# Optimization experiments

Measured on AMD Instinct MI355X. Metric: run time of the kernel, lower is better.

The kernel has to match this reference:

```python
import jax, jax.numpy as jnp
import numpy as np

B, S, D = 8, 2048, 64
NEG = -1e9


def setup_inputs() -> dict:
    key = jax.random.key(0)
    kq, kk, kv = jax.random.split(key, 3)
    return {
        "queries": jax.random.normal(kq, (B, S, D), dtype=jnp.float32),
        "keys": jax.random.normal(kk, (B, S, D), dtype=jnp.float32),
        "values": jax.random.normal(kv, (B, S, D), dtype=jnp.float32),
        "mask_q": jnp.ones((B, S), dtype=jnp.float32),
        "mask_k": jnp.ones((B, S), dtype=jnp.float32),
        "mask_v": jnp.ones((B, S), dtype=jnp.float32),
    }


def reference(queries, keys, values, mask_q, mask_k, mask_v):
    # scaled QK^T: [B, Sq, Sk]
    scaler = jnp.sqrt(jnp.asarray(queries.shape[-1], dtype=queries.dtype))
    scores = jnp.einsum("bqd,bkd->bqk", queries, keys) / scaler
    # additive padding mask from outer product of query/key masks
    padding_mask = mask_q[:, :, None] * mask_k[:, None, :]  # [B, Sq, Sk]
    scores = scores + (1.0 - padding_mask) * NEG
    attention_weights = jax.nn.softmax(scores, axis=-1)
    # mask values then weighted sum
    values = values * mask_v[:, :, None]
    output = jnp.einsum("bqk,bkd->bqd", attention_weights, values)
    return output
```

## Files before the change

kernel.cpp:

```cpp
#include <hip/hip_runtime.h>
#include <hip/hip_bf16.h>
#include <math.h>

#define BATCH 8
#define SEQ   2048
#define DIM   64
#define NEGC  (-1e9f)

typedef short short8  __attribute__((ext_vector_type(8)));
typedef float f32x4   __attribute__((ext_vector_type(4)));
typedef float f32x16  __attribute__((ext_vector_type(16)));

#define MFMA32(a, b, c) __builtin_amdgcn_mfma_f32_32x32x16_bf16((a), (b), (c), 0, 0, 0)

__device__ __forceinline__ ushort f2bf(float x) {
    uint u = __float_as_uint(x);
    uint r = (u + 0x7fffu + ((u >> 16) & 1u)) >> 16;
    return (ushort)r;
}
__device__ __forceinline__ float bf2f(ushort h) {
    return __uint_as_float(((uint)h) << 16);
}

__global__ __launch_bounds__(256)
void prep_kv(const float* __restrict__ K, const float* __restrict__ V,
             const float* __restrict__ MV, ushort* __restrict__ ws) {
    __shared__ float raw[64 * 68];
    const int t    = threadIdx.x;
    const int b    = blockIdx.x >> 5;
    const int tile = blockIdx.x & 31;
    const float* Kb  = K  + ((size_t)b * SEQ + tile * 64) * DIM;
    const float* Vb  = V  + ((size_t)b * SEQ + tile * 64) * DIM;
    const float* MVb = MV + (size_t)b * SEQ + tile * 64;
    ushort* wsI = ws + (size_t)(b * 32 + tile) * 8192;

#pragma unroll
    for (int u = 0; u < 4; u++) {
        int f = t + 256 * u, key = f >> 4, d4 = (f & 15) * 4;
        *(float4*)&raw[key * 68 + d4] = *(const float4*)(Kb + (size_t)f * 4);
    }
    __syncthreads();
#pragma unroll
    for (int u = 0; u < 2; u++) {
        int r = t + 256 * u;
        int mt = r >> 8, kc = (r >> 6) & 3, L = r & 63;
        int key = mt * 32 + (L & 31), d0 = kc * 16 + (L >> 5) * 8;
        float4 x0 = *(float4*)&raw[key * 68 + d0];
        float4 x1 = *(float4*)&raw[key * 68 + d0 + 4];
        float xs[8] = {x0.x, x0.y, x0.z, x0.w, x1.x, x1.y, x1.z, x1.w};
        short8 hv;
#pragma unroll
        for (int j = 0; j < 8; j++) hv[j] = (short)f2bf(xs[j]);
        *(short8*)(wsI + r * 8) = hv;
    }
    __syncthreads();

#pragma unroll
    for (int u = 0; u < 4; u++) {
        int f = t + 256 * u, key = f >> 4, d4 = (f & 15) * 4;
        float4 x = *(const float4*)(Vb + (size_t)f * 4);
        float mv = MVb[key];
        x.x *= mv; x.y *= mv; x.z *= mv; x.w *= mv;
        *(float4*)&raw[key * 68 + d4] = x;
    }
    __syncthreads();
#pragma unroll
    for (int u = 0; u < 2; u++) {
        int r = t + 256 * u;
        int dt = r >> 8, kc = (r >> 6) & 3, L = r & 63;
        int d = dt * 32 + (L & 31), k0 = kc * 16 + (L >> 5) * 8;
        short8 ov;
#pragma unroll
        for (int j = 0; j < 8; j++) ov[j] = (short)f2bf(raw[(k0 + j) * 68 + d]);
        *(short8*)(wsI + 4096 + r * 8) = ov;
    }
}

__global__ __launch_bounds__(256, 2)
void attn_main(const float* __restrict__ Q, const float* __restrict__ MQ,
               const float* __restrict__ MK, const ushort* __restrict__ ws,
               float* __restrict__ PO, float* __restrict__ ML) {
    __shared__ __align__(16) ushort Stage[2][8192];
    __shared__ __align__(16) float  Msc[2][64 * 34];

    const int t    = threadIdx.x;
    const int w    = t >> 6;
    const int lane = t & 63;
    const int h    = lane >> 5;
    const int lm   = lane & 31;
    const int qg   = w & 1;
    const int kh   = w >> 1;

    const int s  = blockIdx.x & 1;
    const int qb = blockIdx.x >> 1;
    const int b  = qb >> 5;
    const int qt = qb & 31;
    const int q  = qt * 64 + qg * 32 + lm;

    const float*  MKb  = MK + (size_t)b * SEQ;
    const ushort* wsKV = ws + (size_t)b * 32 * 8192;

    short8 qh[4], ql[4];
    {
        const float* Qr = Q + ((size_t)b * SEQ + q) * DIM;
#pragma unroll
        for (int kc = 0; kc < 4; kc++) {
            const float* p = Qr + kc * 16 + h * 8;
            float4 x0 = *(const float4*)p;
            float4 x1 = *(const float4*)(p + 4);
            float xs[8] = {x0.x, x0.y, x0.z, x0.w, x1.x, x1.y, x1.z, x1.w};
#pragma unroll
            for (int j = 0; j < 8; j++) {
                float v   = xs[j] * 0.125f;
                ushort hi = f2bf(v);
                ql[kc][j] = (short)f2bf(v - bf2f(hi));
                qh[kc][j] = (short)hi;
            }
        }
    }
    const float mq   = MQ[(size_t)b * SEQ + q];
    const float apen = NEGC * mq;

    float m = -1e30f, l = 0.0f;
    f32x16 ot0, ot1;
#pragma unroll
    for (int i = 0; i < 16; i++) { ot0[i] = 0.0f; ot1[i] = 0.0f; }

    {
        const ushort* src = wsKV + (size_t)(s * 16) * 8192;
#pragma unroll
        for (int u = 0; u < 4; u++) {
            const int off = (u * 256 + w * 64 + lane) * 8;
            __builtin_amdgcn_global_load_lds(
                (const __attribute__((address_space(1))) void*)(src + off),
                (__attribute__((address_space(3))) void*)(&Stage[0][0] + off),
                16, 0, 0);
        }
    }
    __syncthreads();

    f32x4 mk[4];
#pragma unroll
    for (int v = 0; v < 4; v++)
        mk[v] = *(const f32x4*)(MKb + (s * 16) * 64 + kh * 32 + v * 8 + h * 4);

#pragma unroll 1
    for (int tt = 0; tt < 16; tt++) {
        const ushort* cur = &Stage[tt & 1][0];

        if (tt + 1 < 16) {
            const ushort* src = wsKV + (size_t)(s * 16 + tt + 1) * 8192;
            ushort* dst = &Stage[(tt + 1) & 1][0];
#pragma unroll
            for (int u = 0; u < 4; u++) {
                const int off = (u * 256 + w * 64 + lane) * 8;
                __builtin_amdgcn_global_load_lds(
                    (const __attribute__((address_space(1))) void*)(src + off),
                    (__attribute__((address_space(3))) void*)(dst + off),
                    16, 0, 0);
            }
        }
        f32x4 nmk[4];
#pragma unroll
        for (int v = 0; v < 4; v++) nmk[v] = mk[v];
        if (tt + 1 < 16) {
            const float* mkp = MKb + (s * 16 + tt + 1) * 64 + kh * 32 + h * 4;
#pragma unroll
            for (int v = 0; v < 4; v++) nmk[v] = *(const f32x4*)(mkp + v * 8);
        }

        f32x16 st;
#pragma unroll
        for (int i = 0; i < 16; i++) st[i] = 0.0f;
#pragma unroll
        for (int kc = 0; kc < 4; kc++) {
            short8 a = *(const short8*)&cur[((kh * 4 + kc) * 64 + lane) * 8];
            st = MFMA32(a, qh[kc], st);
            st = MFMA32(a, ql[kc], st);
        }

        float sv[16];
#pragma unroll
        for (int v = 0; v < 4; v++)
#pragma unroll
            for (int c = 0; c < 4; c++)
                sv[v * 4 + c] = st[v * 4 + c] + (NEGC - apen * mk[v][c]);
        float cm = sv[0];
#pragma unroll
        for (int i = 1; i < 16; i++) cm = fmaxf(cm, sv[i]);
        cm = fmaxf(cm, __shfl_xor(cm, 32));
        float nm    = fmaxf(m, cm);
        float alpha = __expf(m - nm);
        m = nm;

        float p[16], cs = 0.0f;
#pragma unroll
        for (int i = 0; i < 16; i++) { p[i] = __expf(sv[i] - nm); cs += p[i]; }
        cs += __shfl_xor(cs, 32);
        l   = l * alpha + cs;
        ot0 *= alpha; ot1 *= alpha;

        uint g[4][2], x[4][2];
#pragma unroll
        for (int v = 0; v < 4; v++) {
            __hip_bfloat162 c0 = __float22bfloat162_rn(make_float2(p[v*4+0], p[v*4+1]));
            __hip_bfloat162 c1 = __float22bfloat162_rn(make_float2(p[v*4+2], p[v*4+3]));
            __builtin_memcpy(&g[v][0], &c0, 4);
            __builtin_memcpy(&g[v][1], &c1, 4);
            x[v][0] = (uint)__shfl_xor((int)g[v][0], 32);
            x[v][1] = (uint)__shfl_xor((int)g[v][1], 32);
        }
        uint pbw[2][4];
        pbw[0][0] = h ? x[1][0] : g[0][0];
        pbw[0][1] = h ? x[1][1] : g[0][1];
        pbw[0][2] = h ? g[1][0] : x[0][0];
        pbw[0][3] = h ? g[1][1] : x[0][1];
        pbw[1][0] = h ? x[3][0] : g[2][0];
        pbw[1][1] = h ? x[3][1] : g[2][1];
        pbw[1][2] = h ? g[3][0] : x[2][0];
        pbw[1][3] = h ? g[3][1] : x[2][1];

#pragma unroll
        for (int c = 0; c < 2; c++) {
            short8 pb;
            __builtin_memcpy(&pb, &pbw[c][0], 16);
            short8 v0 = *(const short8*)&cur[4096 + ((0 * 4 + kh * 2 + c) * 64 + lane) * 8];
            short8 v1 = *(const short8*)&cur[4096 + ((1 * 4 + kh * 2 + c) * 64 + lane) * 8];
            ot0 = MFMA32(v0, pb, ot0);
            ot1 = MFMA32(v1, pb, ot1);
        }

#pragma unroll
        for (int v = 0; v < 4; v++) mk[v] = nmk[v];
        __syncthreads();
    }

    if (kh == 1) {
        float* sc = &Msc[qg][lane * 34];
#pragma unroll
        for (int i = 0; i < 16; i++) { sc[i] = ot0[i]; sc[16 + i] = ot1[i]; }
        sc[32] = m;
        sc[33] = l;
    }
    __syncthreads();
    if (kh == 0) {
        const float* sc = &Msc[qg][lane * 34];
        float mb = sc[32], lb = sc[33];
        float nm = fmaxf(m, mb);
        float fa = __expf(m - nm);
        float fb = __expf(mb - nm);
        float lt = l * fa + lb * fb;

        float* po = PO + (((size_t)(s * 8 + b) * 32 + qt) * 64 + qg * 32 + lm) * 64;
#pragma unroll
        for (int dt = 0; dt < 2; dt++) {
            const f32x16& o = dt ? ot1 : ot0;
#pragma unroll
            for (int rq = 0; rq < 4; rq++) {
                f32x4 r;
#pragma unroll
                for (int c = 0; c < 4; c++)
                    r[c] = o[rq * 4 + c] * fa + sc[dt * 16 + rq * 4 + c] * fb;
                *(f32x4*)(po + dt * 32 + rq * 8 + h * 4) = r;
            }
        }
        if (h == 0) {
            float2* ml2 = (float2*)ML;
            ml2[((size_t)(s * 8 + b) * 32 + qt) * 64 + qg * 32 + lm] =
                make_float2(nm, lt);
        }
    }
}

__global__ __launch_bounds__(256)
void merge_o(const float* __restrict__ PO, const float* __restrict__ ML,
             float* __restrict__ O) {
    const int tid = blockIdx.x * 256 + threadIdx.x;
    const int qln = tid >> 4;
    const int dq  = tid & 15;
    const int b   = qln >> 11;
    const int qr  = qln & 2047;
    const int qt  = qr >> 6;
    const int qq  = qr & 63;

    const float2* ml2 = (const float2*)ML;
    const size_t mlidx = ((size_t)b * 32 + qt) * 64 + qq;
    float2 A = ml2[mlidx];
    float2 Bv = ml2[(size_t)8 * 32 * 64 + mlidx];
    float mm = fmaxf(A.x, Bv.x);
    float fa = __expf(A.x - mm);
    float fb = __expf(Bv.x - mm);
    float inv = 1.0f / (A.y * fa + Bv.y * fb);

    const size_t o0 = (((size_t)b * 32 + qt) * 64 + qq) * 64 + dq * 4;
    f32x4 va = *(const f32x4*)(PO + o0);
    f32x4 vb = *(const f32x4*)(PO + (size_t)8 * 32 * 64 * 64 + o0);
    f32x4 r = (va * fa + vb * fb) * inv;
    *(f32x4*)(O + ((size_t)b * SEQ + qr) * DIM + dq * 4) = r;
}

extern "C" void kernel_launch(void* const* d_in, const int* in_sizes, int n_in,
                              void* d_out, int out_size, void* d_ws, size_t ws_size,
                              hipStream_t stream) {
    const float* Q  = (const float*)d_in[0];
    const float* K  = (const float*)d_in[1];
    const float* V  = (const float*)d_in[2];
    const float* MQ = (const float*)d_in[3];
    const float* MK = (const float*)d_in[4];
    const float* MV = (const float*)d_in[5];
    float* O = (float*)d_out;

    ushort* wsKV = (ushort*)d_ws;
    float*  PO   = (float*)((char*)d_ws + (4u << 20));
    float*  ML   = (float*)((char*)d_ws + (12u << 20));

    prep_kv  <<<dim3(256),  dim3(256), 0, stream>>>(K, V, MV, wsKV);
    attn_main<<<dim3(512),  dim3(256), 0, stream>>>(Q, MQ, MK, wsKV, PO, ML);
    merge_o  <<<dim3(1024), dim3(256), 0, stream>>>(PO, ML, O);
}
```

Measured before the change: 102.3 us.

## Fuse split-K merge into attention kernel with 4-way in-block key split

Replaces the two-block split over keys plus the separate merge kernel with a single 512-thread block per query tile. Its 8 waves split the keys four ways, and the partial results are merged through LDS before writing the output directly. K/V fragments now load straight from global into registers with a ping-pong prefetch instead of LDS staging with per-tile barriers. It also skips the rescale when the row max does not change and raises wave priority around the MFMAs. The grid drops to 256 blocks, so occupancy and global load latency hiding may suffer.

New measurement: 95.76 us. 6.4% less time.

```diff
diff --git a/kernel.cpp b/kernel.cpp
--- a/kernel.cpp
+++ b/kernel.cpp
@@ -76,12 +76,12 @@
     }
 }
 
-__global__ __launch_bounds__(256, 2)
-void attn_main(const float* __restrict__ Q, const float* __restrict__ MQ,
-               const float* __restrict__ MK, const ushort* __restrict__ ws,
-               float* __restrict__ PO, float* __restrict__ ML) {
-    __shared__ __align__(16) ushort Stage[2][8192];
-    __shared__ __align__(16) float  Msc[2][64 * 34];
+__global__ __launch_bounds__(512, 2)
+void attn_fused(const float* __restrict__ Q, const float* __restrict__ MQ,
+                const float* __restrict__ MK, const ushort* __restrict__ ws,
+                float* __restrict__ O) {
+    __shared__ __align__(16) float Msc[2][3][64][36];
+    __shared__ __align__(16) float Oout[2][32][72];
 
     const int t    = threadIdx.x;
     const int w    = t >> 6;
@@ -89,16 +89,14 @@
     const int h    = lane >> 5;
     const int lm   = lane & 31;
     const int qg   = w & 1;
-    const int kh   = w >> 1;
-
-    const int s  = blockIdx.x & 1;
-    const int qb = blockIdx.x >> 1;
-    const int b  = qb >> 5;
-    const int qt = qb & 31;
+    const int ks   = w >> 1;
+
+    const int b  = blockIdx.x & 7;
+    const int qt = blockIdx.x >> 3;
     const int q  = qt * 64 + qg * 32 + lm;
 
-    const float*  MKb  = MK + (size_t)b * SEQ;
-    const ushort* wsKV = ws + (size_t)b * 32 * 8192;
+    const float*  MKb = MK + (size_t)b * SEQ;
+    const ushort* wsB = ws + (size_t)b * 32 * 8192;
 
     short8 qh[4], ql[4];
     {
@@ -126,79 +124,61 @@
 #pragma unroll
     for (int i = 0; i < 16; i++) { ot0[i] = 0.0f; ot1[i] = 0.0f; }
 
-    {
-        const ushort* src = wsKV + (size_t)(s * 16) * 8192;
+    auto loadch = [&](short8 (&kf)[4], short8 (&vf)[4], f32x4 (&bias)[4], int ch) {
+        const int tt = ch >> 1, mt = ch & 1;
+        const ushort* img = wsB + (size_t)tt * 8192;
+#pragma unroll
+        for (int kc = 0; kc < 4; kc++)
+            kf[kc] = *(const short8*)(img + (((mt * 4 + kc) << 6) + lane) * 8);
 #pragma unroll
         for (int u = 0; u < 4; u++) {
-            const int off = (u * 256 + w * 64 + lane) * 8;
-            __builtin_amdgcn_global_load_lds(
-                (const __attribute__((address_space(1))) void*)(src + off),
-                (__attribute__((address_space(3))) void*)(&Stage[0][0] + off),
-                16, 0, 0);
-        }
-    }
-    __syncthreads();
-
-    f32x4 mk[4];
-#pragma unroll
-    for (int v = 0; v < 4; v++)
-        mk[v] = *(const f32x4*)(MKb + (s * 16) * 64 + kh * 32 + v * 8 + h * 4);
-
-#pragma unroll 1
-    for (int tt = 0; tt < 16; tt++) {
-        const ushort* cur = &Stage[tt & 1][0];
-
-        if (tt + 1 < 16) {
-            const ushort* src = wsKV + (size_t)(s * 16 + tt + 1) * 8192;
-            ushort* dst = &Stage[(tt + 1) & 1][0];
-#pragma unroll
-            for (int u = 0; u < 4; u++) {
-                const int off = (u * 256 + w * 64 + lane) * 8;
-                __builtin_amdgcn_global_load_lds(
-                    (const __attribute__((address_space(1))) void*)(src + off),
-                    (__attribute__((address_space(3))) void*)(dst + off),
-                    16, 0, 0);
-            }
-        }
-        f32x4 nmk[4];
-#pragma unroll
-        for (int v = 0; v < 4; v++) nmk[v] = mk[v];
-        if (tt + 1 < 16) {
-            const float* mkp = MKb + (s * 16 + tt + 1) * 64 + kh * 32 + h * 4;
-#pragma unroll
-            for (int v = 0; v < 4; v++) nmk[v] = *(const f32x4*)(mkp + v * 8);
-        }
-
+            const int dt = u >> 1, c = u & 1;
+            vf[u] = *(const short8*)(img + 4096 + (((dt * 4 + mt * 2 + c) << 6) + lane) * 8);
+        }
+        const float* mkp = MKb + ch * 32 + h * 4;
+#pragma unroll
+        for (int v = 0; v < 4; v++) {
+            f32x4 mk = *(const f32x4*)(mkp + v * 8);
+#pragma unroll
+            for (int c = 0; c < 4; c++) bias[v][c] = NEGC - apen * mk[c];
+        }
+    };
+
+    auto step = [&](const short8 (&kf)[4], const short8 (&vf)[4],
+                    const f32x4 (&bias)[4]) {
         f32x16 st;
 #pragma unroll
         for (int i = 0; i < 16; i++) st[i] = 0.0f;
+        __builtin_amdgcn_s_setprio(1);
 #pragma unroll
         for (int kc = 0; kc < 4; kc++) {
-            short8 a = *(const short8*)&cur[((kh * 4 + kc) * 64 + lane) * 8];
-            st = MFMA32(a, qh[kc], st);
-            st = MFMA32(a, ql[kc], st);
-        }
+            st = MFMA32(kf[kc], qh[kc], st);
+            st = MFMA32(kf[kc], ql[kc], st);
+        }
+        __builtin_amdgcn_s_setprio(0);
 
         float sv[16];
 #pragma unroll
         for (int v = 0; v < 4; v++)
 #pragma unroll
             for (int c = 0; c < 4; c++)
-                sv[v * 4 + c] = st[v * 4 + c] + (NEGC - apen * mk[v][c]);
+                sv[v * 4 + c] = st[v * 4 + c] + bias[v][c];
         float cm = sv[0];
 #pragma unroll
         for (int i = 1; i < 16; i++) cm = fmaxf(cm, sv[i]);
         cm = fmaxf(cm, __shfl_xor(cm, 32));
-        float nm    = fmaxf(m, cm);
-        float alpha = __expf(m - nm);
-        m = nm;
-
+        if (!__all(cm <= m)) {
+            float nm    = fmaxf(m, cm);
+            float alpha = __expf(m - nm);
+            m = nm;
+            l *= alpha;
+            ot0 *= alpha; ot1 *= alpha;
+        }
         float p[16], cs = 0.0f;
 #pragma unroll
-        for (int i = 0; i < 16; i++) { p[i] = __expf(sv[i] - nm); cs += p[i]; }
+        for (int i = 0; i < 16; i++) { p[i] = __expf(sv[i] - m); cs += p[i]; }
         cs += __shfl_xor(cs, 32);
-        l   = l * alpha + cs;
-        ot0 *= alpha; ot1 *= alpha;
+        l += cs;
 
         uint g[4][2], x[4][2];
 #pragma unroll
@@ -220,83 +200,80 @@
         pbw[1][2] = h ? g[3][0] : x[2][0];
         pbw[1][3] = h ? g[3][1] : x[2][1];
 
+        __builtin_amdgcn_s_setprio(1);
 #pragma unroll
         for (int c = 0; c < 2; c++) {
             short8 pb;
             __builtin_memcpy(&pb, &pbw[c][0], 16);
-            short8 v0 = *(const short8*)&cur[4096 + ((0 * 4 + kh * 2 + c) * 64 + lane) * 8];
-            short8 v1 = *(const short8*)&cur[4096 + ((1 * 4 + kh * 2 + c) * 64 + lane) * 8];
-            ot0 = MFMA32(v0, pb, ot0);
-            ot1 = MFMA32(v1, pb, ot1);
-        }
-
-#pragma unroll
-        for (int v = 0; v < 4; v++) mk[v] = nmk[v];
-        __syncthreads();
-    }
-
-    if (kh == 1) {
-        float* sc = &Msc[qg][lane * 34];
-#pragma unroll
-        for (int i = 0; i < 16; i++) { sc[i] = ot0[i]; sc[16 + i] = ot1[i]; }
+            ot0 = MFMA32(vf[c],     pb, ot0);
+            ot1 = MFMA32(vf[2 + c], pb, ot1);
+        }
+        __builtin_amdgcn_s_setprio(0);
+    };
+
+    short8 kA[4], vA[4], kB[4], vB[4];
+    f32x4  bA[4], bB[4];
+    const int ch0 = ks * 16;
+    loadch(kA, vA, bA, ch0);
+#pragma unroll 1
+    for (int i = 0; i < 8; i++) {
+        loadch(kB, vB, bB, ch0 + 2 * i + 1);
+        step(kA, vA, bA);
+        if (i < 7) loadch(kA, vA, bA, ch0 + 2 * i + 2);
+        step(kB, vB, bB);
+    }
+
+    if (ks != 0) {
+        float* sc = &Msc[qg][ks - 1][lane][0];
+#pragma unroll
+        for (int i = 0; i < 4; i++) {
+            f32x4 r0, r1;
+#pragma unroll
+            for (int c = 0; c < 4; c++) { r0[c] = ot0[i*4+c]; r1[c] = ot1[i*4+c]; }
+            *(f32x4*)&sc[i * 4]      = r0;
+            *(f32x4*)&sc[16 + i * 4] = r1;
+        }
         sc[32] = m;
         sc[33] = l;
     }
     __syncthreads();
-    if (kh == 0) {
-        const float* sc = &Msc[qg][lane * 34];
-        float mb = sc[32], lb = sc[33];
-        float nm = fmaxf(m, mb);
-        float fa = __expf(m - nm);
-        float fb = __expf(mb - nm);
-        float lt = l * fa + lb * fb;
-
-        float* po = PO + (((size_t)(s * 8 + b) * 32 + qt) * 64 + qg * 32 + lm) * 64;
-#pragma unroll
-        for (int dt = 0; dt < 2; dt++) {
-            const f32x16& o = dt ? ot1 : ot0;
+    if (ks == 0) {
+#pragma unroll
+        for (int pp = 0; pp < 3; pp++) {
+            const float* sc = &Msc[qg][pp][lane][0];
+            float mb = sc[32], lb = sc[33];
+            float nm = fmaxf(m, mb);
+            float fa = __expf(m - nm), fb = __expf(mb - nm);
+            m = nm;
+            l = l * fa + lb * fb;
+#pragma unroll
+            for (int i = 0; i < 16; i++) {
+                ot0[i] = ot0[i] * fa + sc[i] * fb;
+                ot1[i] = ot1[i] * fa + sc[16 + i] * fb;
+            }
+        }
+        const float inv = 1.0f / l;
+#pragma unroll
+        for (int dt = 0; dt < 2; dt++)
 #pragma unroll
             for (int rq = 0; rq < 4; rq++) {
                 f32x4 r;
 #pragma unroll
                 for (int c = 0; c < 4; c++)
-                    r[c] = o[rq * 4 + c] * fa + sc[dt * 16 + rq * 4 + c] * fb;
-                *(f32x4*)(po + dt * 32 + rq * 8 + h * 4) = r;
+                    r[c] = (dt ? ot1[rq * 4 + c] : ot0[rq * 4 + c]) * inv;
+                *(f32x4*)&Oout[qg][lm][dt * 32 + rq * 8 + h * 4] = r;
             }
-        }
-        if (h == 0) {
-            float2* ml2 = (float2*)ML;
-            ml2[((size_t)(s * 8 + b) * 32 + qt) * 64 + qg * 32 + lm] =
-                make_float2(nm, lt);
-        }
-    }
-}
-
-__global__ __launch_bounds__(256)
-void merge_o(const float* __restrict__ PO, const float* __restrict__ ML,
-             float* __restrict__ O) {
-    const int tid = blockIdx.x * 256 + threadIdx.x;
-    const int qln = tid >> 4;
-    const int dq  = tid & 15;
-    const int b   = qln >> 11;
-    const int qr  = qln & 2047;
-    const int qt  = qr >> 6;
-    const int qq  = qr & 63;
-
-    const float2* ml2 = (const float2*)ML;
-    const size_t mlidx = ((size_t)b * 32 + qt) * 64 + qq;
-    float2 A = ml2[mlidx];
-    float2 Bv = ml2[(size_t)8 * 32 * 64 + mlidx];
-    float mm = fmaxf(A.x, Bv.x);
-    float fa = __expf(A.x - mm);
-    float fb = __expf(Bv.x - mm);
-    float inv = 1.0f / (A.y * fa + Bv.y * fb);
-
-    const size_t o0 = (((size_t)b * 32 + qt) * 64 + qq) * 64 + dq * 4;
-    f32x4 va = *(const f32x4*)(PO + o0);
-    f32x4 vb = *(const f32x4*)(PO + (size_t)8 * 32 * 64 * 64 + o0);
-    f32x4 r = (va * fa + vb * fb) * inv;
-    *(f32x4*)(O + ((size_t)b * SEQ + qr) * DIM + dq * 4) = r;
+    }
+    __syncthreads();
+
+    float* Ob = O + ((size_t)b * SEQ + qt * 64) * DIM;
+#pragma unroll
+    for (int u = 0; u < 2; u++) {
+        int f = t + 512 * u;
+        int row = f >> 4, d4 = (f & 15) * 4;
+        f32x4 val = *(const f32x4*)&Oout[row >> 5][row & 31][d4];
+        *(f32x4*)(Ob + (size_t)row * DIM + d4) = val;
+    }
 }
 
 extern "C" void kernel_launch(void* const* d_in, const int* in_sizes, int n_in,
@@ -311,10 +288,7 @@
     float* O = (float*)d_out;
 
     ushort* wsKV = (ushort*)d_ws;
-    float*  PO   = (float*)((char*)d_ws + (4u << 20));
-    float*  ML   = (float*)((char*)d_ws + (12u << 20));
-
-    prep_kv  <<<dim3(256),  dim3(256), 0, stream>>>(K, V, MV, wsKV);
-    attn_main<<<dim3(512),  dim3(256), 0, stream>>>(Q, MQ, MK, wsKV, PO, ML);
-    merge_o  <<<dim3(1024), dim3(256), 0, stream>>>(PO, ML, O);
-}
+
+    prep_kv   <<<dim3(256), dim3(256), 0, stream>>>(K, V, MV, wsKV);
+    attn_fused<<<dim3(256), dim3(512), 0, stream>>>(Q, MQ, MK, wsKV, O);
+}
```
